# Kernel tuning notes

Hardware: AMD Instinct MI355X
Metric: run time of the kernel (lower is better)

The kernel has to match this reference:

```python
import jax, jax.numpy as jnp
import numpy as np

EMBED = 768
HEADS = 12
HEAD_DIM = EMBED // HEADS  # 64
SCALE = float(EMBED) ** 0.5  # NOTE: module scales by sqrt(embed_size), not sqrt(head_dim)


def setup_inputs() -> dict:
    key = jax.random.key(0)
    k_x, k_wqkv, k_bqkv, k_wp, k_bp = jax.random.split(key, 5)
    x = jax.random.normal(k_x, (16, 1024, EMBED), dtype=jnp.float32)
    # nn.Linear(embed, 3*embed): weight [out,in], bias [out]
    w_qkv = jax.random.normal(k_wqkv, (3 * EMBED, EMBED), dtype=jnp.float32) * 0.02
    b_qkv = jax.random.normal(k_bqkv, (3 * EMBED,), dtype=jnp.float32) * 0.02
    w_proj = jax.random.normal(k_wp, (EMBED, EMBED), dtype=jnp.float32) * 0.02
    b_proj = jax.random.normal(k_bp, (EMBED,), dtype=jnp.float32) * 0.02
    return {"x": x, "w_qkv": w_qkv, "b_qkv": b_qkv, "w_proj": w_proj, "b_proj": b_proj}


def reference(x, w_qkv, b_qkv, w_proj, b_proj):
    B, N, C = x.shape
    qkv = x @ w_qkv.T + b_qkv                       # [B, N, 3C]
    # rearrange 'b n (h d qkv) -> qkv b h n d': qkv index is INNERMOST factor
    qkv = qkv.reshape(B, N, HEADS, HEAD_DIM, 3)
    q = jnp.transpose(qkv[..., 0], (0, 2, 1, 3))    # [B, H, N, D]
    k = jnp.transpose(qkv[..., 1], (0, 2, 1, 3))
    v = jnp.transpose(qkv[..., 2], (0, 2, 1, 3))
    attn = jnp.einsum('bhqd,bhkd->bhqk', q, k) / SCALE
    attn = jax.nn.softmax(attn, axis=-1)
    out = jnp.einsum('bhqk,bhkd->bhqd', attn, v)    # [B, H, N, D]
    out = jnp.transpose(out, (0, 2, 1, 3)).reshape(B, N, C)
    return out @ w_proj.T + b_proj
```

## Files before the change

### kernel.cpp

```cpp
#include <hip/hip_runtime.h>

typedef short bf16x8 __attribute__((ext_vector_type(8)));
typedef float f32x4 __attribute__((ext_vector_type(4)));
typedef float f32x16 __attribute__((ext_vector_type(16)));

#define Q_PRESCALE 0.05205877485199535f

__device__ __forceinline__ unsigned short f2bf(float f) {
  unsigned u = __float_as_uint(f);
  u += 0x7fffu + ((u >> 16) & 1u);
  return (unsigned short)(u >> 16);
}

__device__ __forceinline__ int cvt_pk_bf16(float lo, float hi) {
  int r;
  asm("v_cvt_pk_bf16_f32 %0, %1, %2" : "=v"(r) : "v"(lo), "v"(hi));
  return r;
}

__device__ __forceinline__ float fast_exp2(float x) {
  return __builtin_amdgcn_exp2f(x);
}

__device__ __forceinline__ float cross_half_add(float x) {
  float y;
  asm("v_mov_b32 %0, %1" : "=v"(y) : "v"(x));
  asm("v_permlane32_swap_b32 %0, %1" : "+v"(x), "+v"(y));
  return x + y;
}

__device__ __forceinline__ void gload_lds16(const void* g, void* l) {
  __builtin_amdgcn_global_load_lds(
      (const __attribute__((address_space(1))) void*)g,
      (__attribute__((address_space(3))) void*)l, 16, 0, 0);
}

__global__ __launch_bounds__(256) void prep_kernel(
    const float* __restrict__ x, unsigned short* __restrict__ xb,
    const float* __restrict__ w_qkv, unsigned short* __restrict__ wqkvb,
    const float* __restrict__ w_proj, unsigned short* __restrict__ wprojb) {
  const int bid = blockIdx.x;
  if (bid < 12288) {
    int i = bid * 256 + threadIdx.x;
    float4 v = ((const float4*)x)[i];
    int2 o;
    o.x = cvt_pk_bf16(v.x, v.y);
    o.y = cvt_pk_bf16(v.z, v.w);
    *(int2*)((ushort4*)xb + i) = o;
  } else if (bid < 14016) {
    int i = (bid - 12288) * 256 + threadIdx.x;
    int col = i / 192, i4 = i % 192;
    int c = col / 768, rem = col % 768;
    int h = rem >> 6, d = rem & 63;
    int orig = h * 192 + d * 3 + c;
    float4 v = ((const float4*)(w_qkv + (size_t)orig * 768))[i4];
    int2 o;
    o.x = cvt_pk_bf16(v.x, v.y);
    o.y = cvt_pk_bf16(v.z, v.w);
    *(int2*)((ushort4*)(wqkvb + (size_t)col * 768) + i4) = o;
  } else {
    int i = (bid - 14016) * 256 + threadIdx.x;
    float4 v = ((const float4*)w_proj)[i];
    int2 o;
    o.x = cvt_pk_bf16(v.x, v.y);
    o.y = cvt_pk_bf16(v.z, v.w);
    *(int2*)((ushort4*)wprojb + i) = o;
  }
}

template<int EPI, int NT>
__global__ __launch_bounds__(256) void gemm_bt(
    const unsigned short* __restrict__ A,
    const unsigned short* __restrict__ B,
    const float* __restrict__ bias,
    void* __restrict__ out0,
    unsigned short* __restrict__ Kb,
    unsigned short* __restrict__ VTb) {
  constexpr int K = 768;
  __shared__ __align__(16) unsigned short smem[16384];

  const int tid = threadIdx.x;
  const int w = tid >> 6, lane = tid & 63;
  const int g = lane >> 4, qq = lane & 15;
  const int wr = w >> 1, wc = w & 1;

  const int nwg = gridDim.x, chunk = nwg >> 3;
  const int id = blockIdx.x;
  const int id2 = (id & 7) * chunk + (id >> 3);
  const int bx = id2 % NT, by = id2 / NT;
  const int rowb = by * 128;

  const unsigned short* Ab = A + (size_t)rowb * K;
  const unsigned short* Bb = B + (size_t)bx * 128 * K;

  f32x4 acc[4][4];
#pragma unroll
  for (int i = 0; i < 4; i++)
#pragma unroll
    for (int j = 0; j < 4; j++) acc[i][j] = (f32x4){0.f, 0.f, 0.f, 0.f};

  const int j0 = tid, j1 = tid + 256;
  const int l0 = j0 >> 3, s0 = (j0 & 7) ^ (l0 & 7);
  const int l1 = j1 >> 3, s1 = (j1 & 7) ^ (l1 & 7);
  const size_t off0 = (size_t)(2 * l0 + (s0 >> 2)) * K + (s0 & 3) * 8;
  const size_t off1 = (size_t)(2 * l1 + (s1 >> 2)) * K + (s1 & 3) * 8;

  int aoff[4], boff[4];
#pragma unroll
  for (int mi = 0; mi < 4; mi++) {
    int row = wr * 64 + mi * 16 + qq;
    aoff[mi] = (row >> 1) * 128 + (((g + (row & 1) * 4) ^ ((row >> 1) & 7)) * 16);
    row = wc * 64 + mi * 16 + qq;
    boff[mi] = (row >> 1) * 128 + (((g + (row & 1) * 4) ^ ((row >> 1) & 7)) * 16);
  }

  gload_lds16(Ab + off0, &smem[j0 * 8]);
  gload_lds16(Ab + off1, &smem[j1 * 8]);
  gload_lds16(Bb + off0, &smem[8192 + j0 * 8]);
  gload_lds16(Bb + off1, &smem[8192 + j1 * 8]);
  asm volatile("s_waitcnt vmcnt(0)" ::: "memory");
  __syncthreads();

  int bo = 0;
  for (int t = 0; t < 24; ++t) {
    if (t < 23) {
      const int k0 = (t + 1) * 32;
      const int nb = bo ^ 4096;
      gload_lds16(Ab + off0 + k0, &smem[nb + j0 * 8]);
      gload_lds16(Ab + off1 + k0, &smem[nb + j1 * 8]);
      gload_lds16(Bb + off0 + k0, &smem[8192 + nb + j0 * 8]);
      gload_lds16(Bb + off1 + k0, &smem[8192 + nb + j1 * 8]);
    }
    const char* Ap = (const char*)&smem[bo];
    const char* Bp = (const char*)&smem[8192 + bo];
    bf16x8 af[4], bfr[4];
#pragma unroll
    for (int mi = 0; mi < 4; mi++) af[mi] = *(const bf16x8*)(Ap + aoff[mi]);
#pragma unroll
    for (int ni = 0; ni < 4; ni++) bfr[ni] = *(const bf16x8*)(Bp + boff[ni]);
#pragma unroll
    for (int mi = 0; mi < 4; mi++)
#pragma unroll
      for (int ni = 0; ni < 4; ni++)
        acc[mi][ni] = __builtin_amdgcn_mfma_f32_16x16x32_bf16(af[mi], bfr[ni], acc[mi][ni], 0, 0, 0);
    __syncthreads();
    bo ^= 4096;
  }

  if (EPI == 0) {
    const int c = bx / 6;
    const int h0 = (bx % 6) * 2;
    const int b = rowb >> 10, n0 = rowb & 1023;
    if (c < 2) {
      unsigned short* dst = (c == 0) ? (unsigned short*)out0 : Kb;
      const float scale = (c == 0) ? Q_PRESCALE : 1.0f;
      const int h = h0 + wc;
      const size_t bh = (size_t)(b * 12 + h);
#pragma unroll
      for (int ni = 0; ni < 4; ni++) {
        const int d = ni * 16 + qq;
        const float bv = bias[h * 192 + d * 3 + c];
#pragma unroll
        for (int mi = 0; mi < 4; mi++) {
          const int nb = n0 + wr * 64 + mi * 16 + g * 4;
          unsigned short* base = dst + (bh * 1024 + nb) * 64 + d;
          const int p0 = cvt_pk_bf16((acc[mi][ni][0] + bv) * scale,
                                     (acc[mi][ni][1] + bv) * scale);
          const int p1 = cvt_pk_bf16((acc[mi][ni][2] + bv) * scale,
                                     (acc[mi][ni][3] + bv) * scale);
          base[0]   = (unsigned short)p0;
          base[64]  = (unsigned short)((unsigned)p0 >> 16);
          base[128] = (unsigned short)p1;
          base[192] = (unsigned short)((unsigned)p1 >> 16);
        }
      }
    } else {
      unsigned short* vt = smem;
#pragma unroll
      for (int p = 0; p < 2; ++p) {
        __syncthreads();
        if (wc == p) {
#pragma unroll
          for (int ni = 0; ni < 4; ni++) {
            const int d = ni * 16 + qq;
            const float bv = bias[(h0 + p) * 192 + d * 3 + 2];
#pragma unroll
            for (int mi = 0; mi < 4; mi++) {
              int2 pk;
              pk.x = cvt_pk_bf16(acc[mi][ni][0] + bv, acc[mi][ni][1] + bv);
              pk.y = cvt_pk_bf16(acc[mi][ni][2] + bv, acc[mi][ni][3] + bv);
              *(int2*)&vt[d * 136 + wr * 64 + mi * 16 + g * 4] = pk;
            }
          }
        }
        __syncthreads();
        const size_t bhp = (size_t)(b * 12 + h0 + p);
        const int dd = tid >> 2;
#pragma unroll
        for (int j = 0; j < 4; ++j) {
          const int ch = (tid & 3) + j * 4;
          uint4 vv = *(const uint4*)&vt[dd * 136 + ch * 8];
          const int n = n0 + ch * 8;
          const int tile = n >> 6;
          const int ksd = (n >> 4) & 3;
          const int tk = n & 15;
          *(uint4*)&VTb[bhp * 65536 + (size_t)tile * 4096 + ksd * 1024 + dd * 16 + tk] = vv;
        }
      }
    }
  } else {
    float* O = (float*)out0;
    const int colb = bx * 128 + wc * 64;
#pragma unroll
    for (int ni = 0; ni < 4; ni++) {
      const int col = colb + ni * 16 + qq;
      const float bv = bias[col];
#pragma unroll
      for (int mi = 0; mi < 4; mi++)
#pragma unroll
        for (int r = 0; r < 4; r++) {
          const int row = rowb + wr * 64 + mi * 16 + g * 4 + r;
          O[(size_t)row * 768 + col] = acc[mi][ni][r] + bv;
        }
    }
  }
}

__global__ __launch_bounds__(256, 3) void attn_kernel(
    const unsigned short* __restrict__ Qb,
    const unsigned short* __restrict__ Kb,
    const unsigned short* __restrict__ VTb,
    unsigned short* __restrict__ AO) {
  __shared__ unsigned short Klds[4][4096];
  const int tid = threadIdx.x;
  const int w = tid >> 6, lane = tid & 63;
  const int ql = lane & 31, hi = lane >> 5;

  const int bid = blockIdx.x;
  const int xcd = bid & 7, jj = bid >> 3;
  const int bh = xcd * 24 + (jj >> 3);
  const int qb = jj & 7;
  const int b = bh / 12, h = bh % 12;
  const int q0w = qb * 128 + w * 32;

  const unsigned short* Qh = Qb + (size_t)bh * 65536;
  const unsigned short* Kh = Kb + (size_t)bh * 65536;
  const unsigned short* Vh = VTb + (size_t)bh * 65536;

  bf16x8 qf[4];
#pragma unroll
  for (int ks = 0; ks < 4; ++ks)
    qf[ks] = *(const bf16x8*)&Qh[(size_t)(q0w + ql) * 64 + ks * 16 + hi * 8];

  float l_run = 0.f;
  f32x16 o[2];
#pragma unroll
  for (int dt = 0; dt < 2; ++dt)
#pragma unroll
    for (int i = 0; i < 16; ++i) o[dt][i] = 0.f;

  const int j0 = w * 64 + lane;
  const int r0 = j0 >> 3, s0 = j0 & 7;
  const int g0 = s0 ^ (r0 & 7) ^ ((r0 >> 2) & 6);
  const int sx = (ql & 7) ^ ((ql >> 2) & 6);

  int koff[2][4];
#pragma unroll
  for (int tt = 0; tt < 2; ++tt)
#pragma unroll
    for (int ks = 0; ks < 4; ++ks)
      koff[tt][ks] = (tt * 32 + ql) * 128 + (((ks * 2 + hi) ^ sx) * 16);
  int voff[2][4];
#pragma unroll
  for (int dt = 0; dt < 2; ++dt)
#pragma unroll
    for (int ks = 0; ks < 4; ++ks)
      voff[dt][ks] = ks * 1024 + (dt * 32 + ql) * 16 + hi * 8;

  auto stage = [&](int sb, int t0) {
    gload_lds16(Kh + (size_t)(t0 + r0) * 64 + g0 * 8, &Klds[sb][j0 * 8]);
    gload_lds16(Kh + (size_t)(t0 + r0 + 32) * 64 + g0 * 8, &Klds[sb][j0 * 8 + 2048]);
  };

  stage(0, 0);
  stage(1, 64);
  stage(2, 128);

  for (int t = 0; t < 16; ++t) {
    if (t < 14)      asm volatile("s_waitcnt vmcnt(4)" ::: "memory");
    else if (t == 14) asm volatile("s_waitcnt vmcnt(2)" ::: "memory");
    else              asm volatile("s_waitcnt vmcnt(0)" ::: "memory");
    __syncthreads();
    if (t < 13) stage((t + 3) & 3, (t + 3) * 64);

    const char* Kbuf = (const char*)&Klds[t & 3][0];
    const unsigned short* Vt = Vh + t * 4096;

    f32x16 s[2];
    __builtin_amdgcn_s_setprio(1);
#pragma unroll
    for (int tt = 0; tt < 2; ++tt) {
#pragma unroll
      for (int i = 0; i < 16; ++i) s[tt][i] = 0.f;
#pragma unroll
      for (int ks = 0; ks < 4; ++ks) {
        bf16x8 ka = *(const bf16x8*)(Kbuf + koff[tt][ks]);
        s[tt] = __builtin_amdgcn_mfma_f32_32x32x16_bf16(ka, qf[ks], s[tt], 0, 0, 0);
      }
    }
    __builtin_amdgcn_s_setprio(0);

#pragma unroll
    for (int tt = 0; tt < 2; ++tt)
#pragma unroll
      for (int i = 0; i < 16; ++i) s[tt][i] = fast_exp2(s[tt][i]);

    float r16[16];
#pragma unroll
    for (int i = 0; i < 16; ++i) r16[i] = s[0][i] + s[1][i];
    float r8[8];
#pragma unroll
    for (int i = 0; i < 8; ++i) r8[i] = r16[i] + r16[i + 8];
    float r4[4];
#pragma unroll
    for (int i = 0; i < 4; ++i) r4[i] = r8[i] + r8[i + 4];
    float rs = (r4[0] + r4[1]) + (r4[2] + r4[3]);
    l_run += cross_half_add(rs);

    union PU { int i[4]; bf16x8 h; };
    PU pb[4];
#pragma unroll
    for (int g16 = 0; g16 < 4; ++g16) {
      const int tt = g16 >> 1, rb = (g16 & 1) * 8;
      int A0, A1, B0, B1;
      float a0 = s[tt][rb + 0], a1 = s[tt][rb + 1], a2 = s[tt][rb + 2], a3 = s[tt][rb + 3];
      float b0 = s[tt][rb + 4], b1 = s[tt][rb + 5], b2 = s[tt][rb + 6], b3 = s[tt][rb + 7];
      asm("v_cvt_pk_bf16_f32 %0, %1, %2" : "=v"(A0) : "v"(a0), "v"(a1));
      asm("v_cvt_pk_bf16_f32 %0, %1, %2" : "=v"(A1) : "v"(a2), "v"(a3));
      asm("v_cvt_pk_bf16_f32 %0, %1, %2" : "=v"(B0) : "v"(b0), "v"(b1));
      asm("v_cvt_pk_bf16_f32 %0, %1, %2" : "=v"(B1) : "v"(b2), "v"(b3));
      asm("v_permlane32_swap_b32 %0, %1" : "+v"(A0), "+v"(B0));
      asm("v_permlane32_swap_b32 %0, %1" : "+v"(A1), "+v"(B1));
      pb[g16].i[0] = A0; pb[g16].i[1] = A1; pb[g16].i[2] = B0; pb[g16].i[3] = B1;
    }

    bf16x8 vf[2][4];
#pragma unroll
    for (int dt = 0; dt < 2; ++dt)
#pragma unroll
      for (int ks = 0; ks < 4; ++ks)
        vf[dt][ks] = *(const bf16x8*)&Vt[voff[dt][ks]];

    __builtin_amdgcn_s_setprio(1);
#pragma unroll
    for (int dt = 0; dt < 2; ++dt)
#pragma unroll
      for (int ks = 0; ks < 4; ++ks)
        o[dt] = __builtin_amdgcn_mfma_f32_32x32x16_bf16(vf[dt][ks], pb[ks].h, o[dt], 0, 0, 0);
    __builtin_amdgcn_s_setprio(0);
  }

  const float inv_l = 1.0f / l_run;
  unsigned short* aorow = AO + (size_t)(b * 1024 + q0w + ql) * 768 + h * 64 + hi * 4;
#pragma unroll
  for (int dt = 0; dt < 2; ++dt)
#pragma unroll
    for (int p = 0; p < 4; ++p) {
      int2 vv;
      vv.x = cvt_pk_bf16(o[dt][4 * p + 0] * inv_l, o[dt][4 * p + 1] * inv_l);
      vv.y = cvt_pk_bf16(o[dt][4 * p + 2] * inv_l, o[dt][4 * p + 3] * inv_l);
      *(int2*)&aorow[dt * 32 + 8 * p] = vv;
    }
}

extern "C" void kernel_launch(void* const* d_in, const int* in_sizes, int n_in,
                              void* d_out, int out_size, void* d_ws, size_t ws_size,
                              hipStream_t stream) {
  const float* x      = (const float*)d_in[0];
  const float* w_qkv  = (const float*)d_in[1];
  const float* b_qkv  = (const float*)d_in[2];
  const float* w_proj = (const float*)d_in[3];
  const float* b_proj = (const float*)d_in[4];

  char* ws = (char*)d_ws;
  unsigned short* xb     = (unsigned short*)(ws);
  unsigned short* Qb     = (unsigned short*)(ws + 25165824);
  unsigned short* Kb     = (unsigned short*)(ws + 50331648);
  unsigned short* VTb    = (unsigned short*)(ws + 75497472);
  unsigned short* wqkvb  = (unsigned short*)(ws + 100663296);
  unsigned short* wprojb = (unsigned short*)(ws + 104202240);
  unsigned short* AO = xb;

  prep_kernel<<<14592, 256, 0, stream>>>(x, xb, w_qkv, wqkvb, w_proj, wprojb);

  gemm_bt<0, 18><<<2304, 256, 0, stream>>>(xb, wqkvb, b_qkv, (void*)Qb, Kb, VTb);
  attn_kernel<<<1536, 256, 0, stream>>>(Qb, Kb, VTb, AO);
  gemm_bt<1, 6><<<768, 256, 0, stream>>>(AO, wprojb, b_proj, d_out, nullptr, nullptr);
}
```

Measured before the change: 208.4 us.

## Triple-buffer GEMM LDS staging with one barrier per k-step

```diff
diff --git a/kernel.cpp b/kernel.cpp
--- a/kernel.cpp
+++ b/kernel.cpp
@@ -77,7 +77,7 @@
     unsigned short* __restrict__ Kb,
     unsigned short* __restrict__ VTb) {
   constexpr int K = 768;
-  __shared__ __align__(16) unsigned short smem[16384];
+  __shared__ __align__(16) unsigned short smem[24576];
 
   const int tid = threadIdx.x;
   const int w = tid >> 6, lane = tid & 63;
@@ -114,25 +114,25 @@
     boff[mi] = (row >> 1) * 128 + (((g + (row & 1) * 4) ^ ((row >> 1) & 7)) * 16);
   }
 
-  gload_lds16(Ab + off0, &smem[j0 * 8]);
-  gload_lds16(Ab + off1, &smem[j1 * 8]);
-  gload_lds16(Bb + off0, &smem[8192 + j0 * 8]);
-  gload_lds16(Bb + off1, &smem[8192 + j1 * 8]);
-  asm volatile("s_waitcnt vmcnt(0)" ::: "memory");
-  __syncthreads();
-
-  int bo = 0;
+  auto stageg = [&](int sb, int k0) {
+    unsigned short* base = &smem[sb * 8192];
+    gload_lds16(Ab + off0 + k0, base + j0 * 8);
+    gload_lds16(Ab + off1 + k0, base + j1 * 8);
+    gload_lds16(Bb + off0 + k0, base + 4096 + j0 * 8);
+    gload_lds16(Bb + off1 + k0, base + 4096 + j1 * 8);
+  };
+
+  stageg(0, 0);
+  stageg(1, 32);
+
   for (int t = 0; t < 24; ++t) {
-    if (t < 23) {
-      const int k0 = (t + 1) * 32;
-      const int nb = bo ^ 4096;
-      gload_lds16(Ab + off0 + k0, &smem[nb + j0 * 8]);
-      gload_lds16(Ab + off1 + k0, &smem[nb + j1 * 8]);
-      gload_lds16(Bb + off0 + k0, &smem[8192 + nb + j0 * 8]);
-      gload_lds16(Bb + off1 + k0, &smem[8192 + nb + j1 * 8]);
-    }
-    const char* Ap = (const char*)&smem[bo];
-    const char* Bp = (const char*)&smem[8192 + bo];
+    if (t < 23) asm volatile("s_waitcnt vmcnt(4)" ::: "memory");
+    else        asm volatile("s_waitcnt vmcnt(0)" ::: "memory");
+    asm volatile("s_barrier" ::: "memory");
+    if (t < 22) stageg((t + 2) % 3, (t + 2) * 32);
+
+    const char* Ap = (const char*)&smem[(t % 3) * 8192];
+    const char* Bp = Ap + 8192;
     bf16x8 af[4], bfr[4];
 #pragma unroll
     for (int mi = 0; mi < 4; mi++) af[mi] = *(const bf16x8*)(Ap + aoff[mi]);
@@ -143,8 +143,6 @@
 #pragma unroll
       for (int ni = 0; ni < 4; ni++)
         acc[mi][ni] = __builtin_amdgcn_mfma_f32_16x16x32_bf16(af[mi], bfr[ni], acc[mi][ni], 0, 0, 0);
-    __syncthreads();
-    bo ^= 4096;
   }
 
   if (EPI == 0) {
```

Result: faster. 203.1 us (-2.5%).
